# Kernel tuning notes

Hardware: AMD Instinct MI355X
Metric: run time of the kernel (lower is better)

The kernel has to match this reference:

```python
import jax, jax.numpy as jnp
import numpy as np

TOP_K = 2

def setup_inputs() -> dict:
    key = jax.random.key(0)
    ks = jax.random.split(key, 5)
    B, T, C, E, H = 4, 2048, 1024, 16, 4096
    x = jax.random.normal(ks[0], (B, T, C), dtype=jnp.float32)
    w_router = jax.random.normal(ks[1], (C, E), dtype=jnp.float32) / np.sqrt(C)
    w1 = jax.random.normal(ks[2], (E, C, H), dtype=jnp.float32) / np.sqrt(C)
    b1 = jnp.zeros((E, H), dtype=jnp.float32)
    w2 = jax.random.normal(ks[3], (E, H, C), dtype=jnp.float32) / np.sqrt(H)
    b2 = jnp.zeros((E, C), dtype=jnp.float32)
    return {"x": x, "w_router": w_router, "w1": w1, "b1": b1, "w2": w2, "b2": b2}


def reference(x, w_router, w1, b1, w2, b2):
    B, T, C = x.shape
    E = w1.shape[0]
    xf = x.reshape(-1, C)                       # [N, C]
    N = xf.shape[0]

    logits = xf @ w_router                      # [N, E]
    rw, sel = jax.lax.top_k(logits, TOP_K)      # [N, K]
    rw = jax.nn.softmax(rw.astype(jnp.float32), axis=-1).astype(x.dtype)

    # combine weight per (token, expert): sum of routing weights over the
    # k-slots that selected that expert (equivalent to the per-k masked loop)
    comb = jnp.zeros((N, E), dtype=x.dtype)
    comb = comb.at[jnp.arange(N)[:, None], sel].add(rw)  # [N, E]

    # loop over experts via scan: out += comb[:, e:e+1] * FFN_e(xf)
    def step(acc, params):
        w1e, b1e, w2e, b2e, ce = params         # ce: [N]
        h = jax.nn.relu(xf @ w1e + b1e)         # [N, 4C]
        y = h @ w2e + b2e                       # [N, C]
        return acc + ce[:, None] * y, None

    out0 = jnp.zeros_like(xf)
    out, _ = jax.lax.scan(step, out0, (w1, b1, w2, b2, comb.T))
    return out.reshape(B, T, C)
```

## Files before the change

### kernel.cpp

```cpp
#include <hip/hip_runtime.h>
#include <hip/hip_bf16.h>


typedef __attribute__((ext_vector_type(4))) float f32x4;
typedef __attribute__((ext_vector_type(8))) __bf16 bf16x8;
typedef __attribute__((ext_vector_type(8))) unsigned short u16x8;

#define NEXP 16
#define CAP  2048
#define CDIM 1024
#define HDIM 4096
#define KS2 2
#define BMG 256
#define BNG 256
#define SLOT 8192

__device__ __forceinline__ unsigned short f2bf(float f) {
  return __builtin_bit_cast(unsigned short, (__bf16)f);
}

__device__ __forceinline__ void xcd_remap(int& bx, int& by, int& bz) {
  const int gx = gridDim.x, gy = gridDim.y;
  const int nwg = gx * gy * gridDim.z;
  int flat = blockIdx.x + gx * (blockIdx.y + gy * blockIdx.z);
  flat = (flat & 7) * (nwg >> 3) + (flat >> 3);
  bx = flat % gx;
  const int t = flat / gx;
  by = t % gy;
  bz = t / gy;
}

__global__ __launch_bounds__(64) void router_kernel(
    const float* __restrict__ x, const float* __restrict__ wr,
    float* __restrict__ pair_w, int* __restrict__ counts,
    int* __restrict__ lists)
{
  const int n = blockIdx.x;
  const int l = threadIdx.x;
  const float* xrow = x + (size_t)n * CDIM;
  double acc[NEXP];
#pragma unroll
  for (int e = 0; e < NEXP; e++) acc[e] = 0.0;
  for (int it = 0; it < CDIM / 64; it++) {
    const int c = l + it * 64;
    const double xv = (double)xrow[c];
    const float* w = wr + c * NEXP;
#pragma unroll
    for (int e = 0; e < NEXP; e++) acc[e] += xv * (double)w[e];
  }
#pragma unroll
  for (int e = 0; e < NEXP; e++) {
    double v = acc[e];
    for (int off = 32; off > 0; off >>= 1) v += __shfl_xor(v, off, 64);
    acc[e] = v;
  }
  if (l == 0) {
    int e0 = 0; double b0 = acc[0];
    for (int e = 1; e < NEXP; e++) if (acc[e] > b0) { b0 = acc[e]; e0 = e; }
    int e1 = -1; double b1v = -1e300;
    for (int e = 0; e < NEXP; e++) {
      if (e == e0) continue;
      if (acc[e] > b1v) { b1v = acc[e]; e1 = e; }
    }
    const double d = exp(b1v - b0);
    pair_w[2 * n]     = (float)(1.0 / (1.0 + d));
    pair_w[2 * n + 1] = (float)(d / (1.0 + d));
    int p0 = atomicAdd(&counts[e0], 1);
    if (p0 < CAP) lists[e0 * CAP + p0] = 2 * n;
    int p1 = atomicAdd(&counts[e1], 1);
    if (p1 < CAP) lists[e1 * CAP + p1] = 2 * n + 1;
  }
}

__global__ __launch_bounds__(256) void cvt_x_kernel(
    const float* __restrict__ x, unsigned short* __restrict__ xb, int n8)
{
  const int i = blockIdx.x * 256 + threadIdx.x;
  if (i >= n8) return;
  float4 a = ((const float4*)x)[2 * i];
  float4 b = ((const float4*)x)[2 * i + 1];
  u16x8 v;
  v[0] = f2bf(a.x); v[1] = f2bf(a.y); v[2] = f2bf(a.z); v[3] = f2bf(a.w);
  v[4] = f2bf(b.x); v[5] = f2bf(b.y); v[6] = f2bf(b.z); v[7] = f2bf(b.w);
  ((u16x8*)xb)[i] = v;
}

__global__ __launch_bounds__(256) void transpose_cvt_kernel(
    const float* __restrict__ src, unsigned short* __restrict__ dst,
    int K, int Nn)
{
  __shared__ __align__(16) unsigned short tile[64][72];
  const size_t eoff = (size_t)blockIdx.z * K * Nn;
  const float* S = src + eoff;
  unsigned short* D = dst + eoff;
  const int n0 = blockIdx.x * 64, k0 = blockIdx.y * 64;
  const int t = threadIdx.x;
  {
    const int nl = (t & 15) * 4, kr = t >> 4;
#pragma unroll
    for (int p = 0; p < 4; p++) {
      const int k = kr + p * 16;
      float4 v = *(const float4*)(S + (size_t)(k0 + k) * Nn + n0 + nl);
      tile[nl + 0][k] = f2bf(v.x);
      tile[nl + 1][k] = f2bf(v.y);
      tile[nl + 2][k] = f2bf(v.z);
      tile[nl + 3][k] = f2bf(v.w);
    }
  }
  __syncthreads();
  {
    const int kq = (t & 7) * 8, nr = t >> 3;
#pragma unroll
    for (int p = 0; p < 2; p++) {
      const int n = nr + p * 32;
      u16x8 v = *(const u16x8*)&tile[n][kq];
      *(u16x8*)(D + (size_t)(n0 + n) * K + k0 + kq) = v;
    }
  }
}


#define LOADR(ra0, ra1, rb0, rb1, koffb)                                       \
  do {                                                                         \
    ra0 = *(const u16x8*)(ag0 + (koffb));                                      \
    ra1 = *(const u16x8*)(ag1 + (koffb));                                      \
    rb0 = *(const u16x8*)(bg0 + (koffb));                                      \
    rb1 = *(const u16x8*)(bg1 + (koffb));                                      \
  } while (0)

#define DSW(parx, hx, ra0, ra1, rb0, rb1)                                      \
  do {                                                                         \
    unsigned short* SA_ = &lds[((parx) * 2 + (hx)) * SLOT];                    \
    unsigned short* SB_ = &lds[4 * SLOT + ((parx) * 2 + (hx)) * SLOT];         \
    *(u16x8*)(SA_ + sw0) = ra0;                                                \
    *(u16x8*)(SA_ + sw1) = ra1;                                                \
    *(u16x8*)(SB_ + sw0) = rb0;                                                \
    *(u16x8*)(SB_ + sw1) = rb1;                                                \
  } while (0)

#define COMPUTE(parx, hx)                                                      \
  do {                                                                         \
    const unsigned short* As_ = &lds[((parx) * 2 + (hx)) * SLOT];              \
    const unsigned short* Bs_ = &lds[4 * SLOT + ((parx) * 2 + (hx)) * SLOT];   \
    bf16x8 af[8], bfv[4];                                                      \
    _Pragma("unroll")                                                          \
    for (int mf = 0; mf < 8; mf++)                                             \
      af[mf] = *(const bf16x8*)(As_ + (wr * 128 + mf * 16 + lrow) * 32 + qsw); \
    _Pragma("unroll")                                                          \
    for (int nf = 0; nf < 4; nf++)                                             \
      bfv[nf] = *(const bf16x8*)(Bs_ + (wc * 64 + nf * 16 + lrow) * 32 + qsw); \
    __builtin_amdgcn_s_setprio(1);                                             \
    _Pragma("unroll")                                                          \
    for (int mf = 0; mf < 8; mf++)                                             \
      _Pragma("unroll")                                                        \
      for (int nf = 0; nf < 4; nf++)                                           \
        acc[mf][nf] = __builtin_amdgcn_mfma_f32_16x16x32_bf16(                 \
            af[mf], bfv[nf], acc[mf][nf], 0, 0, 0);                            \
    __builtin_amdgcn_s_setprio(0);                                             \
  } while (0)

#define SBAR asm volatile("s_barrier" ::: "memory")

#define GEMM_MAIN_LOOP(NT)                                                     \
  u16x8 eA0, eA1, eB0, eB1, oA0, oA1, oB0, oB1;                                \
  LOADR(eA0, eA1, eB0, eB1, 0);                                                \
  LOADR(oA0, oA1, oB0, oB1, 64);                                               \
  DSW(0, 0, eA0, eA1, eB0, eB1);                                               \
  DSW(0, 1, oA0, oA1, oB0, oB1);                                               \
  LOADR(eA0, eA1, eB0, eB1, 128);                                              \
  LOADR(oA0, oA1, oB0, oB1, 192);                                              \
  asm volatile("s_waitcnt lgkmcnt(0)" ::: "memory");                           \
  for (int tt = 0; tt < (NT); ++tt) {                                          \
    const int par = tt & 1;                                                    \
    SBAR;                                                                      \
    if (tt + 1 < (NT)) DSW(par ^ 1, 0, eA0, eA1, eB0, eB1);                    \
    if (tt + 2 < (NT)) LOADR(eA0, eA1, eB0, eB1, (tt + 2) * 128);              \
    COMPUTE(par, 0);                                                           \
    if (tt + 1 < (NT)) DSW(par ^ 1, 1, oA0, oA1, oB0, oB1);                    \
    if (tt + 2 < (NT)) LOADR(oA0, oA1, oB0, oB1, (tt + 2) * 128 + 64);         \
    COMPUTE(par, 1);                                                           \
  }

__global__ __launch_bounds__(512, 2) void gemm1_8p_kernel(
    const unsigned short* __restrict__ xb, const unsigned short* __restrict__ wb,
    const float* __restrict__ b1, const int* __restrict__ counts,
    const int* __restrict__ lists, unsigned short* __restrict__ Hb)
{
  int bx, by, bz;
  xcd_remap(bx, by, bz);
  const int e = bz;
  int cnt = counts[e]; if (cnt > CAP) cnt = CAP;
  const int m0 = by * BMG;
  if (m0 >= cnt) return;
  const int n0 = bx * BNG;
  const int* list = lists + e * CAP;
  const unsigned short* W = wb + (size_t)e * CDIM * HDIM;

  __shared__ __align__(16) unsigned short lds[8 * SLOT];

  const int t = threadIdx.x, w = t >> 6, lane = t & 63;
  const int wr = w >> 2, wc = w & 3;
  const int lrow = lane & 15, lgrp = lane >> 4;
  const int qsw = (lgrp ^ ((lrow >> 1) & 3)) * 8;

  const int sr0 = w * 16 + (lane >> 2), sr1 = 128 + sr0;
  const int wq = ((lane & 3) ^ ((lane >> 3) & 3)) * 8;
  const int sw0 = sr0 * 32 + wq, sw1 = sr1 * 32 + wq;
  int ai0 = m0 + sr0; if (ai0 > cnt - 1) ai0 = cnt - 1;
  int ai1 = m0 + sr1; if (ai1 > cnt - 1) ai1 = cnt - 1;
  const char* ag0 = (const char*)(xb + (size_t)(list[ai0] >> 1) * CDIM) + (lane & 3) * 16;
  const char* ag1 = (const char*)(xb + (size_t)(list[ai1] >> 1) * CDIM) + (lane & 3) * 16;
  const char* bg0 = (const char*)(W + (size_t)(n0 + sr0) * CDIM) + (lane & 3) * 16;
  const char* bg1 = (const char*)(W + (size_t)(n0 + sr1) * CDIM) + (lane & 3) * 16;

  f32x4 acc[8][4] = {};

  GEMM_MAIN_LOOP(CDIM / 64)

  int hrow[8][4]; bool valid[8][4];
#pragma unroll
  for (int mf = 0; mf < 8; mf++)
#pragma unroll
    for (int rr = 0; rr < 4; rr++) {
      const int mi = m0 + wr * 128 + mf * 16 + lgrp * 4 + rr;
      valid[mf][rr] = (mi < cnt);
      hrow[mf][rr] = list[valid[mf][rr] ? mi : (cnt - 1)];
    }
#pragma unroll
  for (int nf = 0; nf < 4; nf++) {
    const int col = n0 + wc * 64 + nf * 16 + lrow;
    const float bias = b1[e * HDIM + col];
#pragma unroll
    for (int mf = 0; mf < 8; mf++)
#pragma unroll
      for (int rr = 0; rr < 4; rr++)
        if (valid[mf][rr]) {
          float h = acc[mf][nf][rr] + bias;
          h = h > 0.f ? h : 0.f;
          Hb[(size_t)hrow[mf][rr] * HDIM + col] = f2bf(h);
        }
  }
}

__global__ __launch_bounds__(512, 2) void gemm2_8p_kernel(
    const unsigned short* __restrict__ Hb, const unsigned short* __restrict__ wb,
    const float* __restrict__ b2, const float* __restrict__ pair_w,
    const int* __restrict__ counts, const int* __restrict__ lists,
    float* __restrict__ out)
{
  int bx, by, bz;
  xcd_remap(bx, by, bz);
  const int e = bz / KS2, ks = bz % KS2;
  int cnt = counts[e]; if (cnt > CAP) cnt = CAP;
  const int m0 = by * BMG;
  if (m0 >= cnt) return;
  const int n0 = bx * BNG;
  const int* list = lists + e * CAP;
  const unsigned short* W = wb + (size_t)e * HDIM * CDIM;
  const int kbegb = ks * (HDIM / KS2) * 2;

  __shared__ __align__(16) unsigned short lds[8 * SLOT];

  const int t = threadIdx.x, w = t >> 6, lane = t & 63;
  const int wr = w >> 2, wc = w & 3;
  const int lrow = lane & 15, lgrp = lane >> 4;
  const int qsw = (lgrp ^ ((lrow >> 1) & 3)) * 8;

  const int sr0 = w * 16 + (lane >> 2), sr1 = 128 + sr0;
  const int wq = ((lane & 3) ^ ((lane >> 3) & 3)) * 8;
  const int sw0 = sr0 * 32 + wq, sw1 = sr1 * 32 + wq;
  int ai0 = m0 + sr0; if (ai0 > cnt - 1) ai0 = cnt - 1;
  int ai1 = m0 + sr1; if (ai1 > cnt - 1) ai1 = cnt - 1;
  const char* ag0 = (const char*)(Hb + (size_t)list[ai0] * HDIM) + kbegb + (lane & 3) * 16;
  const char* ag1 = (const char*)(Hb + (size_t)list[ai1] * HDIM) + kbegb + (lane & 3) * 16;
  const char* bg0 = (const char*)(W + (size_t)(n0 + sr0) * HDIM) + kbegb + (lane & 3) * 16;
  const char* bg1 = (const char*)(W + (size_t)(n0 + sr1) * HDIM) + kbegb + (lane & 3) * 16;

  f32x4 acc[8][4] = {};

  GEMM_MAIN_LOOP((HDIM / KS2) / 64)

  float wgt[8][4]; int tok[8][4]; bool valid[8][4];
#pragma unroll
  for (int mf = 0; mf < 8; mf++)
#pragma unroll
    for (int rr = 0; rr < 4; rr++) {
      const int mi = m0 + wr * 128 + mf * 16 + lgrp * 4 + rr;
      valid[mf][rr] = (mi < cnt);
      const int p = list[valid[mf][rr] ? mi : (cnt - 1)];
      wgt[mf][rr] = pair_w[p];
      tok[mf][rr] = p >> 1;
    }
#pragma unroll
  for (int nf = 0; nf < 4; nf++) {
    const int col = n0 + wc * 64 + nf * 16 + lrow;
    const float bias = (ks == 0) ? b2[e * CDIM + col] : 0.f;
#pragma unroll
    for (int mf = 0; mf < 8; mf++)
#pragma unroll
      for (int rr = 0; rr < 4; rr++)
        if (valid[mf][rr])
          atomicAdd(out + (size_t)tok[mf][rr] * CDIM + col,
                    wgt[mf][rr] * (acc[mf][nf][rr] + bias));
  }
}

__device__ __forceinline__ int swz(int row, int b) {
  return row * 128 + (b ^ (((row >> 1) & 7) << 4));
}

#define MFMA_COMPUTE_F(Abase, Bbase)                                           \
  _Pragma("unroll")                                                            \
  for (int kk = 0; kk < 2; kk++) {                                             \
    bf16x8 af[4], bfr[4];                                                      \
    const int kb = (kk * 32 + lgrp * 8) * 2;                                   \
    _Pragma("unroll")                                                          \
    for (int i = 0; i < 4; i++)                                                \
      af[i] = *(const bf16x8*)((Abase) + swz(wm + i * 16 + lrow, kb));         \
    _Pragma("unroll")                                                          \
    for (int j = 0; j < 4; j++)                                                \
      bfr[j] = *(const bf16x8*)((Bbase) + swz(wn + j * 16 + lrow, kb));        \
    _Pragma("unroll")                                                          \
    for (int i = 0; i < 4; i++)                                                \
      _Pragma("unroll")                                                        \
      for (int j = 0; j < 4; j++)                                              \
        acc[i][j] = __builtin_amdgcn_mfma_f32_16x16x32_bf16(                   \
            af[i], bfr[j], acc[i][j], 0, 0, 0);                                \
  }

__global__ __launch_bounds__(256) void gemm1_f32_kernel(
    const float* __restrict__ x, const float* __restrict__ w1,
    const float* __restrict__ b1, const int* __restrict__ counts,
    const int* __restrict__ lists, unsigned short* __restrict__ Hb,
    int e_base, int h_by_pair)
{
  const int e = e_base + blockIdx.z;
  int cnt = counts[e]; if (cnt > CAP) cnt = CAP;
  const int m0 = blockIdx.y * 128;
  if (m0 >= cnt) return;
  const int n0 = blockIdx.x * 128;
  const int* list = lists + e * CAP;
  const float* W = w1 + (size_t)e * CDIM * HDIM;
  __shared__ __align__(16) unsigned short As[128 * 64];
  __shared__ __align__(16) unsigned short Bs[128 * 64];
  const int t = threadIdx.x;
  const int a_row = t >> 1, a_half = t & 1;
  int a_idx = m0 + a_row; if (a_idx > cnt - 1) a_idx = cnt - 1;
  const float* a_src = x + (size_t)(list[a_idx] >> 1) * CDIM + a_half * 32;
  const int b_np = t & 63, b_kg = t >> 6;
  const int wid = t >> 6, lane = t & 63;
  const int wm = (wid >> 1) * 64, wn = (wid & 1) * 64;
  const int lrow = lane & 15, lgrp = lane >> 4;
  f32x4 acc[4][4] = {};
  for (int kt = 0; kt < CDIM; kt += 64) {
    {
      const float* s = a_src + kt;
      u16x8 cv[4];
#pragma unroll
      for (int q = 0; q < 4; q++) {
        float4 v0 = *(const float4*)(s + q * 8);
        float4 v1 = *(const float4*)(s + q * 8 + 4);
        cv[q][0] = f2bf(v0.x); cv[q][1] = f2bf(v0.y);
        cv[q][2] = f2bf(v0.z); cv[q][3] = f2bf(v0.w);
        cv[q][4] = f2bf(v1.x); cv[q][5] = f2bf(v1.y);
        cv[q][6] = f2bf(v1.z); cv[q][7] = f2bf(v1.w);
      }
#pragma unroll
      for (int q = 0; q < 4; q++)
        *(u16x8*)((char*)As + swz(a_row, (a_half * 32 + q * 8) * 2)) = cv[q];
    }
    {
#pragma unroll
      for (int it = 0; it < 2; it++) {
        const int k0 = (b_kg + 4 * it) * 8;
        u16x8 c0, c1;
#pragma unroll
        for (int j = 0; j < 8; j++) {
          float2 v = *(const float2*)(W + (size_t)(kt + k0 + j) * HDIM + n0 + 2 * b_np);
          c0[j] = f2bf(v.x); c1[j] = f2bf(v.y);
        }
        *(u16x8*)((char*)Bs + swz(2 * b_np,     k0 * 2)) = c0;
        *(u16x8*)((char*)Bs + swz(2 * b_np + 1, k0 * 2)) = c1;
      }
    }
    __syncthreads();
    MFMA_COMPUTE_F((const char*)As, (const char*)Bs)
    __syncthreads();
  }
  int hrow[4][4]; bool valid[4][4];
#pragma unroll
  for (int i = 0; i < 4; i++)
#pragma unroll
    for (int r = 0; r < 4; r++) {
      const int mi = m0 + wm + i * 16 + lgrp * 4 + r;
      valid[i][r] = (mi < cnt);
      const int idx = valid[i][r] ? mi : (cnt - 1);
      hrow[i][r] = h_by_pair ? list[idx] : idx;
    }
#pragma unroll
  for (int j = 0; j < 4; j++) {
    const int col = n0 + wn + j * 16 + lrow;
    const float bias = b1[e * HDIM + col];
#pragma unroll
    for (int i = 0; i < 4; i++)
#pragma unroll
      for (int r = 0; r < 4; r++)
        if (valid[i][r]) {
          float h = acc[i][j][r] + bias;
          h = h > 0.f ? h : 0.f;
          Hb[(size_t)hrow[i][r] * HDIM + col] = f2bf(h);
        }
  }
}

__global__ __launch_bounds__(256) void gemm2_f32_kernel(
    const unsigned short* __restrict__ Hb, const float* __restrict__ w2,
    const float* __restrict__ b2, const float* __restrict__ pair_w,
    const int* __restrict__ counts, const int* __restrict__ lists,
    float* __restrict__ out, int e_base, int h_by_pair)
{
  const int e = e_base + blockIdx.z;
  int cnt = counts[e]; if (cnt > CAP) cnt = CAP;
  const int m0 = blockIdx.y * 128;
  if (m0 >= cnt) return;
  const int n0 = blockIdx.x * 128;
  const int* list = lists + e * CAP;
  const float* W = w2 + (size_t)e * HDIM * CDIM;
  __shared__ __align__(16) unsigned short As[128 * 64];
  __shared__ __align__(16) unsigned short Bs[128 * 64];
  const int t = threadIdx.x;
  const int a_row = t >> 1, a_half = t & 1;
  int a_idx = m0 + a_row; if (a_idx > cnt - 1) a_idx = cnt - 1;
  const unsigned short* a_src =
      Hb + (size_t)(h_by_pair ? list[a_idx] : a_idx) * HDIM + a_half * 32;
  const int b_np = t & 63, b_kg = t >> 6;
  const int wid = t >> 6, lane = t & 63;
  const int wm = (wid >> 1) * 64, wn = (wid & 1) * 64;
  const int lrow = lane & 15, lgrp = lane >> 4;
  f32x4 acc[4][4] = {};
  for (int kt = 0; kt < HDIM; kt += 64) {
    {
      const unsigned short* s = a_src + kt;
#pragma unroll
      for (int q = 0; q < 4; q++) {
        u16x8 v = *(const u16x8*)(s + q * 8);
        *(u16x8*)((char*)As + swz(a_row, (a_half * 32 + q * 8) * 2)) = v;
      }
    }
    {
#pragma unroll
      for (int it = 0; it < 2; it++) {
        const int k0 = (b_kg + 4 * it) * 8;
        u16x8 c0, c1;
#pragma unroll
        for (int j = 0; j < 8; j++) {
          float2 v = *(const float2*)(W + (size_t)(kt + k0 + j) * CDIM + n0 + 2 * b_np);
          c0[j] = f2bf(v.x); c1[j] = f2bf(v.y);
        }
        *(u16x8*)((char*)Bs + swz(2 * b_np,     k0 * 2)) = c0;
        *(u16x8*)((char*)Bs + swz(2 * b_np + 1, k0 * 2)) = c1;
      }
    }
    __syncthreads();
    MFMA_COMPUTE_F((const char*)As, (const char*)Bs)
    __syncthreads();
  }
  float wgt[4][4]; int tok[4][4]; bool valid[4][4];
#pragma unroll
  for (int i = 0; i < 4; i++)
#pragma unroll
    for (int r = 0; r < 4; r++) {
      const int mi = m0 + wm + i * 16 + lgrp * 4 + r;
      valid[i][r] = (mi < cnt);
      const int idx = valid[i][r] ? mi : (cnt - 1);
      const int p = list[idx];
      wgt[i][r] = pair_w[p];
      tok[i][r] = p >> 1;
    }
#pragma unroll
  for (int j = 0; j < 4; j++) {
    const int col = n0 + wn + j * 16 + lrow;
    const float bias = b2[e * CDIM + col];
#pragma unroll
    for (int i = 0; i < 4; i++)
#pragma unroll
      for (int r = 0; r < 4; r++)
        if (valid[i][r])
          atomicAdd(out + (size_t)tok[i][r] * CDIM + col,
                    wgt[i][r] * (acc[i][j][r] + bias));
  }
}

extern "C" void kernel_launch(void* const* d_in, const int* in_sizes, int n_in,
                              void* d_out, int out_size, void* d_ws, size_t ws_size,
                              hipStream_t stream)
{
  const float* x  = (const float*)d_in[0];
  const float* wr = (const float*)d_in[1];
  const float* w1 = (const float*)d_in[2];
  const float* b1 = (const float*)d_in[3];
  const float* w2 = (const float*)d_in[4];
  const float* b2 = (const float*)d_in[5];
  float* out = (float*)d_out;

  const int N = in_sizes[0] / CDIM;

  char* ws = (char*)d_ws;
  int* counts = (int*)ws;
  int* lists  = (int*)(ws + 256);
  float* pw   = (float*)(ws + 256 + NEXP * CAP * 4);
  size_t off = 256 + (size_t)NEXP * CAP * 4 + (size_t)2 * N * 4;
  off = (off + 255) & ~(size_t)255;
  unsigned short* xb = (unsigned short*)(ws + off);
  const size_t xb_sz = (size_t)N * CDIM * 2;
  unsigned short* Hb = (unsigned short*)(ws + off + xb_sz);
  const size_t Hb_sz = (size_t)2 * N * HDIM * 2;
  unsigned short* wb = (unsigned short*)(ws + off + xb_sz + Hb_sz);
  const size_t wb_sz = (size_t)NEXP * CDIM * HDIM * 2;

  const size_t need_new = off + xb_sz + Hb_sz + wb_sz;
  const size_t need_old = off + Hb_sz;

  hipMemsetAsync(d_ws, 0, 64, stream);
  hipMemsetAsync(d_out, 0, (size_t)out_size * 4, stream);

  router_kernel<<<N, 64, 0, stream>>>(x, wr, pw, counts, lists);

  if (ws_size >= need_new) {
    cvt_x_kernel<<<(N * CDIM / 8 + 255) / 256, 256, 0, stream>>>(
        x, xb, N * CDIM / 8);
    transpose_cvt_kernel<<<dim3(HDIM / 64, CDIM / 64, NEXP), 256, 0, stream>>>(
        w1, wb, CDIM, HDIM);
    gemm1_8p_kernel<<<dim3(HDIM / BNG, CAP / BMG, NEXP), 512, 0, stream>>>(
        xb, wb, b1, counts, lists, Hb);
    transpose_cvt_kernel<<<dim3(CDIM / 64, HDIM / 64, NEXP), 256, 0, stream>>>(
        w2, wb, HDIM, CDIM);
    gemm2_8p_kernel<<<dim3(CDIM / BNG, CAP / BMG, NEXP * KS2), 512, 0, stream>>>(
        Hb, wb, b2, pw, counts, lists, out);
  } else if (ws_size >= need_old) {
    unsigned short* Hb0 = (unsigned short*)(ws + off);
    gemm1_f32_kernel<<<dim3(HDIM / 128, CAP / 128, NEXP), 256, 0, stream>>>(
        x, w1, b1, counts, lists, Hb0, 0, 1);
    gemm2_f32_kernel<<<dim3(CDIM / 128, CAP / 128, NEXP), 256, 0, stream>>>(
        Hb0, w2, b2, pw, counts, lists, out, 0, 1);
  }
}
```

Measured before the change: 948.7 us.

## Fuse fp32 weight conversion into GEMM loads and x conversion into router

Drops the separate transpose/convert passes that produced bf16 transposed copies of w1 and w2. The GEMM kernels now read fp32 weights directly with strided scalar loads, convert them to bf16 in registers and write them to LDS. The x-to-bf16 conversion is folded into the router kernel. This removes large extra read/write passes over the weights and two kernel launches. In exchange each GEMM tile reads fp32 weights (twice the bytes) with narrower loads and converts in the inner loop, and weight tiles are re-read by every M-block. The fallback path now has the router write bf16 x into Hb0, which is probably harmless since gemm1 overwrites that buffer afterward.

```diff
diff --git a/kernel.cpp b/kernel.cpp
--- a/kernel.cpp
+++ b/kernel.cpp
@@ -33,17 +33,20 @@
 __global__ __launch_bounds__(64) void router_kernel(
     const float* __restrict__ x, const float* __restrict__ wr,
     float* __restrict__ pair_w, int* __restrict__ counts,
-    int* __restrict__ lists)
+    int* __restrict__ lists, unsigned short* __restrict__ xb)
 {
   const int n = blockIdx.x;
   const int l = threadIdx.x;
   const float* xrow = x + (size_t)n * CDIM;
+  unsigned short* xbrow = xb + (size_t)n * CDIM;
   double acc[NEXP];
 #pragma unroll
   for (int e = 0; e < NEXP; e++) acc[e] = 0.0;
   for (int it = 0; it < CDIM / 64; it++) {
     const int c = l + it * 64;
-    const double xv = (double)xrow[c];
+    const float xf = xrow[c];
+    xbrow[c] = f2bf(xf);
+    const double xv = (double)xf;
     const float* w = wr + c * NEXP;
 #pragma unroll
     for (int e = 0; e < NEXP; e++) acc[e] += xv * (double)w[e];
@@ -72,70 +75,44 @@
   }
 }
 
-__global__ __launch_bounds__(256) void cvt_x_kernel(
-    const float* __restrict__ x, unsigned short* __restrict__ xb, int n8)
-{
-  const int i = blockIdx.x * 256 + threadIdx.x;
-  if (i >= n8) return;
-  float4 a = ((const float4*)x)[2 * i];
-  float4 b = ((const float4*)x)[2 * i + 1];
-  u16x8 v;
-  v[0] = f2bf(a.x); v[1] = f2bf(a.y); v[2] = f2bf(a.z); v[3] = f2bf(a.w);
-  v[4] = f2bf(b.x); v[5] = f2bf(b.y); v[6] = f2bf(b.z); v[7] = f2bf(b.w);
-  ((u16x8*)xb)[i] = v;
-}
-
-__global__ __launch_bounds__(256) void transpose_cvt_kernel(
-    const float* __restrict__ src, unsigned short* __restrict__ dst,
-    int K, int Nn)
-{
-  __shared__ __align__(16) unsigned short tile[64][72];
-  const size_t eoff = (size_t)blockIdx.z * K * Nn;
-  const float* S = src + eoff;
-  unsigned short* D = dst + eoff;
-  const int n0 = blockIdx.x * 64, k0 = blockIdx.y * 64;
-  const int t = threadIdx.x;
-  {
-    const int nl = (t & 15) * 4, kr = t >> 4;
-#pragma unroll
-    for (int p = 0; p < 4; p++) {
-      const int k = kr + p * 16;
-      float4 v = *(const float4*)(S + (size_t)(k0 + k) * Nn + n0 + nl);
-      tile[nl + 0][k] = f2bf(v.x);
-      tile[nl + 1][k] = f2bf(v.y);
-      tile[nl + 2][k] = f2bf(v.z);
-      tile[nl + 3][k] = f2bf(v.w);
-    }
-  }
-  __syncthreads();
-  {
-    const int kq = (t & 7) * 8, nr = t >> 3;
-#pragma unroll
-    for (int p = 0; p < 2; p++) {
-      const int n = nr + p * 32;
-      u16x8 v = *(const u16x8*)&tile[n][kq];
-      *(u16x8*)(D + (size_t)(n0 + n) * K + k0 + kq) = v;
-    }
-  }
-}
-
-
-#define LOADR(ra0, ra1, rb0, rb1, koffb)                                       \
+
+#define LOADA(kbyte)                                                           \
   do {                                                                         \
-    ra0 = *(const u16x8*)(ag0 + (koffb));                                      \
-    ra1 = *(const u16x8*)(ag1 + (koffb));                                      \
-    rb0 = *(const u16x8*)(bg0 + (koffb));                                      \
-    rb1 = *(const u16x8*)(bg1 + (koffb));                                      \
+    rA0 = *(const u16x8*)(ag0 + (kbyte));                                      \
+    rA1 = *(const u16x8*)(ag1 + (kbyte));                                      \
+    rA2 = *(const u16x8*)(ag0 + (kbyte) + 64);                                 \
+    rA3 = *(const u16x8*)(ag1 + (kbyte) + 64);                                 \
   } while (0)
 
-#define DSW(parx, hx, ra0, ra1, rb0, rb1)                                      \
+#define DSWA(parx)                                                             \
   do {                                                                         \
-    unsigned short* SA_ = &lds[((parx) * 2 + (hx)) * SLOT];                    \
-    unsigned short* SB_ = &lds[4 * SLOT + ((parx) * 2 + (hx)) * SLOT];         \
-    *(u16x8*)(SA_ + sw0) = ra0;                                                \
-    *(u16x8*)(SA_ + sw1) = ra1;                                                \
-    *(u16x8*)(SB_ + sw0) = rb0;                                                \
-    *(u16x8*)(SB_ + sw1) = rb1;                                                \
+    unsigned short* S0_ = &lds[((parx) * 2 + 0) * SLOT];                       \
+    unsigned short* S1_ = &lds[((parx) * 2 + 1) * SLOT];                       \
+    *(u16x8*)(S0_ + sw0) = rA0;                                                \
+    *(u16x8*)(S0_ + sw1) = rA1;                                                \
+    *(u16x8*)(S1_ + sw0) = rA2;                                                \
+    *(u16x8*)(S1_ + sw1) = rA3;                                                \
+  } while (0)
+
+#define LOADB(ktv)                                                             \
+  do {                                                                         \
+    _Pragma("unroll")                                                          \
+    for (int u = 0; u < 4; u++)                                                \
+      _Pragma("unroll")                                                        \
+      for (int j = 0; j < 8; j++)                                              \
+        rB[u][j] = bgu[u][(size_t)((ktv) + j) * BNN];                          \
+  } while (0)
+
+#define DSWB(parx)                                                             \
+  do {                                                                         \
+    unsigned short* SB_ = &lds[4 * SLOT + ((parx) * 2 + bh) * SLOT];           \
+    _Pragma("unroll")                                                          \
+    for (int u = 0; u < 4; u++) {                                              \
+      u16x8 v_;                                                                \
+      _Pragma("unroll")                                                        \
+      for (int j = 0; j < 8; j++) v_[j] = f2bf(rB[u][j]);                      \
+      *(u16x8*)(SB_ + brow * 32 + (u ^ bqx) * 8) = v_;                         \
+    }                                                                          \
   } while (0)
 
 #define COMPUTE(parx, hx)                                                      \
@@ -162,27 +139,22 @@
 #define SBAR asm volatile("s_barrier" ::: "memory")
 
 #define GEMM_MAIN_LOOP(NT)                                                     \
-  u16x8 eA0, eA1, eB0, eB1, oA0, oA1, oB0, oB1;                                \
-  LOADR(eA0, eA1, eB0, eB1, 0);                                                \
-  LOADR(oA0, oA1, oB0, oB1, 64);                                               \
-  DSW(0, 0, eA0, eA1, eB0, eB1);                                               \
-  DSW(0, 1, oA0, oA1, oB0, oB1);                                               \
-  LOADR(eA0, eA1, eB0, eB1, 128);                                              \
-  LOADR(oA0, oA1, oB0, oB1, 192);                                              \
+  u16x8 rA0, rA1, rA2, rA3; float rB[4][8];                                    \
+  LOADA(0); LOADB(0);                                                          \
+  DSWA(0); DSWB(0);                                                            \
+  LOADA(128); LOADB(64);                                                       \
   asm volatile("s_waitcnt lgkmcnt(0)" ::: "memory");                           \
   for (int tt = 0; tt < (NT); ++tt) {                                          \
     const int par = tt & 1;                                                    \
     SBAR;                                                                      \
-    if (tt + 1 < (NT)) DSW(par ^ 1, 0, eA0, eA1, eB0, eB1);                    \
-    if (tt + 2 < (NT)) LOADR(eA0, eA1, eB0, eB1, (tt + 2) * 128);              \
+    if (tt + 1 < (NT)) { DSWA(par ^ 1); DSWB(par ^ 1); }                       \
+    if (tt + 2 < (NT)) { LOADA((tt + 2) * 128); LOADB((tt + 2) * 64); }        \
     COMPUTE(par, 0);                                                           \
-    if (tt + 1 < (NT)) DSW(par ^ 1, 1, oA0, oA1, oB0, oB1);                    \
-    if (tt + 2 < (NT)) LOADR(oA0, oA1, oB0, oB1, (tt + 2) * 128 + 64);         \
     COMPUTE(par, 1);                                                           \
   }
 
 __global__ __launch_bounds__(512, 2) void gemm1_8p_kernel(
-    const unsigned short* __restrict__ xb, const unsigned short* __restrict__ wb,
+    const unsigned short* __restrict__ xb, const float* __restrict__ w1f,
     const float* __restrict__ b1, const int* __restrict__ counts,
     const int* __restrict__ lists, unsigned short* __restrict__ Hb)
 {
@@ -194,7 +166,8 @@
   if (m0 >= cnt) return;
   const int n0 = bx * BNG;
   const int* list = lists + e * CAP;
-  const unsigned short* W = wb + (size_t)e * CDIM * HDIM;
+  const float* Wf = w1f + (size_t)e * CDIM * HDIM;
+  const int BNN = HDIM;
 
   __shared__ __align__(16) unsigned short lds[8 * SLOT];
 
@@ -210,8 +183,12 @@
   int ai1 = m0 + sr1; if (ai1 > cnt - 1) ai1 = cnt - 1;
   const char* ag0 = (const char*)(xb + (size_t)(list[ai0] >> 1) * CDIM) + (lane & 3) * 16;
   const char* ag1 = (const char*)(xb + (size_t)(list[ai1] >> 1) * CDIM) + (lane & 3) * 16;
-  const char* bg0 = (const char*)(W + (size_t)(n0 + sr0) * CDIM) + (lane & 3) * 16;
-  const char* bg1 = (const char*)(W + (size_t)(n0 + sr1) * CDIM) + (lane & 3) * 16;
+
+  const int brow = t & 255, bh = t >> 8, bqx = (brow >> 1) & 3;
+  const float* bgu[4];
+#pragma unroll
+  for (int u = 0; u < 4; u++)
+    bgu[u] = Wf + (size_t)(bh * 32 + u * 8) * BNN + n0 + brow;
 
   f32x4 acc[8][4] = {};
 
@@ -243,7 +220,7 @@
 }
 
 __global__ __launch_bounds__(512, 2) void gemm2_8p_kernel(
-    const unsigned short* __restrict__ Hb, const unsigned short* __restrict__ wb,
+    const unsigned short* __restrict__ Hb, const float* __restrict__ w2f,
     const float* __restrict__ b2, const float* __restrict__ pair_w,
     const int* __restrict__ counts, const int* __restrict__ lists,
     float* __restrict__ out)
@@ -256,8 +233,9 @@
   if (m0 >= cnt) return;
   const int n0 = bx * BNG;
   const int* list = lists + e * CAP;
-  const unsigned short* W = wb + (size_t)e * HDIM * CDIM;
-  const int kbegb = ks * (HDIM / KS2) * 2;
+  const float* Wf = w2f + (size_t)e * HDIM * CDIM;
+  const int BNN = CDIM;
+  const int kbeg = ks * (HDIM / KS2);
 
   __shared__ __align__(16) unsigned short lds[8 * SLOT];
 
@@ -271,10 +249,14 @@
   const int sw0 = sr0 * 32 + wq, sw1 = sr1 * 32 + wq;
   int ai0 = m0 + sr0; if (ai0 > cnt - 1) ai0 = cnt - 1;
   int ai1 = m0 + sr1; if (ai1 > cnt - 1) ai1 = cnt - 1;
-  const char* ag0 = (const char*)(Hb + (size_t)list[ai0] * HDIM) + kbegb + (lane & 3) * 16;
-  const char* ag1 = (const char*)(Hb + (size_t)list[ai1] * HDIM) + kbegb + (lane & 3) * 16;
-  const char* bg0 = (const char*)(W + (size_t)(n0 + sr0) * HDIM) + kbegb + (lane & 3) * 16;
-  const char* bg1 = (const char*)(W + (size_t)(n0 + sr1) * HDIM) + kbegb + (lane & 3) * 16;
+  const char* ag0 = (const char*)(Hb + (size_t)list[ai0] * HDIM + kbeg) + (lane & 3) * 16;
+  const char* ag1 = (const char*)(Hb + (size_t)list[ai1] * HDIM + kbeg) + (lane & 3) * 16;
+
+  const int brow = t & 255, bh = t >> 8, bqx = (brow >> 1) & 3;
+  const float* bgu[4];
+#pragma unroll
+  for (int u = 0; u < 4; u++)
+    bgu[u] = Wf + (size_t)(kbeg + bh * 32 + u * 8) * BNN + n0 + brow;
 
   f32x4 acc[8][4] = {};
 
@@ -515,30 +497,22 @@
   const size_t xb_sz = (size_t)N * CDIM * 2;
   unsigned short* Hb = (unsigned short*)(ws + off + xb_sz);
   const size_t Hb_sz = (size_t)2 * N * HDIM * 2;
-  unsigned short* wb = (unsigned short*)(ws + off + xb_sz + Hb_sz);
-  const size_t wb_sz = (size_t)NEXP * CDIM * HDIM * 2;
-
-  const size_t need_new = off + xb_sz + Hb_sz + wb_sz;
+
+  const size_t need_new = off + xb_sz + Hb_sz;
   const size_t need_old = off + Hb_sz;
 
   hipMemsetAsync(d_ws, 0, 64, stream);
   hipMemsetAsync(d_out, 0, (size_t)out_size * 4, stream);
 
-  router_kernel<<<N, 64, 0, stream>>>(x, wr, pw, counts, lists);
-
   if (ws_size >= need_new) {
-    cvt_x_kernel<<<(N * CDIM / 8 + 255) / 256, 256, 0, stream>>>(
-        x, xb, N * CDIM / 8);
-    transpose_cvt_kernel<<<dim3(HDIM / 64, CDIM / 64, NEXP), 256, 0, stream>>>(
-        w1, wb, CDIM, HDIM);
+    router_kernel<<<N, 64, 0, stream>>>(x, wr, pw, counts, lists, xb);
     gemm1_8p_kernel<<<dim3(HDIM / BNG, CAP / BMG, NEXP), 512, 0, stream>>>(
-        xb, wb, b1, counts, lists, Hb);
-    transpose_cvt_kernel<<<dim3(CDIM / 64, HDIM / 64, NEXP), 256, 0, stream>>>(
-        w2, wb, HDIM, CDIM);
+        xb, w1, b1, counts, lists, Hb);
     gemm2_8p_kernel<<<dim3(CDIM / BNG, CAP / BMG, NEXP * KS2), 512, 0, stream>>>(
-        Hb, wb, b2, pw, counts, lists, out);
+        Hb, w2, b2, pw, counts, lists, out);
   } else if (ws_size >= need_old) {
     unsigned short* Hb0 = (unsigned short*)(ws + off);
+    router_kernel<<<N, 64, 0, stream>>>(x, wr, pw, counts, lists, Hb0);
     gemm1_f32_kernel<<<dim3(HDIM / 128, CAP / 128, NEXP), 256, 0, stream>>>(
         x, w1, b1, counts, lists, Hb0, 0, 1);
     gemm2_f32_kernel<<<dim3(CDIM / 128, CAP / 128, NEXP), 256, 0, stream>>>(
```

After: 876.7 us. -7.6%, faster.
